# Optimization experiments

Hardware: AMD Instinct MI355X
Metric: run time of the kernel (lower is better)

## Reference

```python
import jax, jax.numpy as jnp
import numpy as np
import math

V, B, S, D, H, DH, DMEM = 32000, 4, 1024, 1024, 16, 64, 16
HD = H * DH  # == D (required by ff: Linear(n_head*d_head, d_model))
SCALE = 1.0 / math.sqrt(DH)


def pos_table(max_len, d):
    pos = jnp.arange(max_len, dtype=jnp.float32)[:, None]
    freqs = jnp.power(10000.0, -jnp.arange(0, d, 2, dtype=jnp.float32) / d)
    tab = jnp.zeros((max_len, d), dtype=jnp.float32)
    tab = tab.at[:, 0::2].set(jnp.sin(pos * freqs))
    tab = tab.at[:, 1::2].set(jnp.cos(pos * freqs))
    return tab


def layer_norm(x, g, b, eps=1e-5):
    mu = x.mean(-1, keepdims=True)
    var = ((x - mu) ** 2).mean(-1, keepdims=True)
    return (x - mu) * jax.lax.rsqrt(var + eps) * g + b


def mha(h, c, qw, kvw, ow, g, b):
    # h: [B,Sq,D] queries; c: [B,Skv,D] key/value source (post-lnorm, no mask, eval mode)
    q = (h @ qw).reshape(h.shape[0], h.shape[1], H, DH)
    k, v = jnp.split(c @ kvw, 2, axis=-1)
    k = k.reshape(c.shape[0], c.shape[1], H, DH)
    v = v.reshape(c.shape[0], c.shape[1], H, DH)
    scores = jnp.einsum('bind,bjnd->bijn', q, k) * SCALE
    probs = jax.nn.softmax(scores, axis=2)  # softmax over key axis j
    vec = jnp.einsum('bijn,bjnd->bind', probs, v).reshape(h.shape[0], h.shape[1], HD)
    return layer_norm(h + vec @ ow, g, b)


def setup_inputs():
    key = jax.random.key(0)
    ks = jax.random.split(key, 16)
    w = lambda k, shape: jax.random.normal(k, shape, dtype=jnp.float32) * 0.02
    ones = lambda: jnp.ones((D,), dtype=jnp.float32)
    zeros = lambda: jnp.zeros((D,), dtype=jnp.float32)
    return {
        'data': jax.random.randint(ks[0], (B, S), 0, V, dtype=jnp.int32),
        'mem': jnp.zeros((B, DMEM, D), dtype=jnp.float32),
        'emb': w(ks[1], (V, D)),
        'a_qw': w(ks[2], (D, HD)), 'a_kvw': w(ks[3], (D, 2 * HD)), 'a_ow': w(ks[4], (HD, D)),
        'a_g': ones(), 'a_b': zeros(),
        'u_qw': w(ks[5], (D, HD)), 'u_kvw': w(ks[6], (D, 2 * HD)), 'u_ow': w(ks[7], (HD, D)),
        'u_g': ones(), 'u_b': zeros(),
        'ffu_w': w(ks[8], (HD, D)), 'lnu_g': ones(), 'lnu_b': zeros(),
        'o_qw': w(ks[9], (D, HD)), 'o_kvw': w(ks[10], (D, 2 * HD)), 'o_ow': w(ks[11], (HD, D)),
        'o_g': ones(), 'o_b': zeros(),
        'ff2_w': w(ks[12], (HD, D)), 'ln1_g': ones(), 'ln1_b': zeros(),
        'ln2_g': ones(), 'ln2_b': zeros(),
    }


def reference(data, mem, emb, a_qw, a_kvw, a_ow, a_g, a_b,
              u_qw, u_kvw, u_ow, u_g, u_b, ffu_w, lnu_g, lnu_b,
              o_qw, o_kvw, o_ow, o_g, o_b, ff2_w, ln1_g, ln1_b, ln2_g, ln2_b):
    pos = pos_table(S, D)[None, :, :]  # [1,S,D]
    # embedding scale + sinusoidal positional encoding (dropout=0 in eval)
    hids = emb[data] * math.sqrt(D) + pos
    # layer self-attention (post-lnorm residual)
    hids = mha(hids, hids, a_qw, a_kvw, a_ow, a_g, a_b)
    # UpdateAttn: queries from hids, kv over [mem; hids]
    u = mha(hids, jnp.concatenate([mem, hids], axis=1), u_qw, u_kvw, u_ow, u_g, u_b)
    u = u + u @ ffu_w          # output += self.ff(output)
    u = layer_norm(u, lnu_g, lnu_b)
    u = u + (u + pos)          # output += pos_emb(output)
    # memory rollover: keep last d_mem positions of [new_mem; hids]
    new_mem = jnp.concatenate([u, hids], axis=1)[:, -DMEM:, :]
    # OutputAttn: hids attend over [new_mem; hids]
    attn_out = mha(hids, jnp.concatenate([new_mem, hids], axis=1), o_qw, o_kvw, o_ow, o_g, o_b)
    out_attn = layer_norm(hids + attn_out, ln1_g, ln1_b)
    output = layer_norm(out_attn @ ff2_w + out_attn, ln2_g, ln2_b)
    return (output, new_mem)
```

## Files before the change

kernel.cpp:

```cpp
#include <hip/hip_runtime.h>
#include <hip/hip_bf16.h>
#include <math.h>

typedef __bf16 bf16;
typedef __bf16 bf16x4 __attribute__((ext_vector_type(4)));
typedef __bf16 bf16x8 __attribute__((ext_vector_type(8)));
typedef float floatx4 __attribute__((ext_vector_type(4)));

#define LOG2E 1.44269504088896340736f
#define AS1 __attribute__((address_space(1)))
#define AS3 __attribute__((address_space(3)))

__device__ __forceinline__ void async_g2l16(const bf16* g, bf16* l) {
  __builtin_amdgcn_global_load_lds((AS1 void*)(void*)g, (AS3 void*)(void*)l, 16, 0, 0);
}

__global__ __launch_bounds__(256) void embed_kernel(const int* __restrict__ data,
                                                    const float* __restrict__ emb,
                                                    bf16* __restrict__ out) {
  int row = blockIdx.x;
  int s = row & 1023;
  int tok = data[row];
  int d = threadIdx.x * 4;
  floatx4 ev = *(const floatx4*)(emb + (size_t)tok * 1024 + d);
  bf16x4 ov;
#pragma unroll
  for (int i = 0; i < 4; i++) {
    int di = d + i;
    float e = -(float)(di & ~1) * (13.287712379549449f / 1024.0f);
    float freq = exp2f(e);
    float ang = (float)s * freq;
    float pv = (di & 1) ? cosf(ang) : sinf(ang);
    ov[i] = (bf16)(ev[i] * 32.0f + pv);
  }
  *(bf16x4*)(out + (size_t)row * 1024 + d) = ov;
}

__global__ __launch_bounds__(256) void transpose_kernel(const float* __restrict__ src,
                                                        bf16* __restrict__ dst,
                                                        int R, int C) {
  __shared__ __align__(16) bf16 tile[64][72];
  int c0 = blockIdx.x * 64, r0 = blockIdx.y * 64;
  int t = threadIdx.x;
  int r = t >> 2, cg = (t & 3) * 16;
  const float* sp = src + (size_t)(r0 + r) * C + c0 + cg;
  floatx4 f0 = *(const floatx4*)sp;
  floatx4 f1 = *(const floatx4*)(sp + 4);
  floatx4 f2 = *(const floatx4*)(sp + 8);
  floatx4 f3 = *(const floatx4*)(sp + 12);
  bf16x8 v0, v1;
#pragma unroll
  for (int i = 0; i < 4; i++) {
    v0[i] = (bf16)f0[i];
    v0[4 + i] = (bf16)f1[i];
    v1[i] = (bf16)f2[i];
    v1[4 + i] = (bf16)f3[i];
  }
  *(bf16x8*)&tile[r][cg] = v0;
  *(bf16x8*)&tile[r][cg + 8] = v1;
  __syncthreads();
  bf16x8 o0, o1;
#pragma unroll
  for (int i = 0; i < 8; i++) o0[i] = tile[cg + i][r];
#pragma unroll
  for (int i = 0; i < 8; i++) o1[i] = tile[cg + 8 + i][r];
  bf16* dp = dst + (size_t)(c0 + r) * R + r0 + cg;
  *(bf16x8*)dp = o0;
  *(bf16x8*)(dp + 8) = o1;
}

template <int EPI, int MT>
__global__ __launch_bounds__(256) void gemm_kernel(const bf16* __restrict__ A,
                                                   const bf16* __restrict__ Bt,
                                                   bf16* __restrict__ C0,
                                                   bf16* __restrict__ C1,
                                                   bf16* __restrict__ Vt, int N) {
  constexpr int NJ = (MT == 128) ? 4 : 2;
  constexpr int PA = MT / 32;
  __shared__ __align__(16) bf16 As[MT * 64];
  __shared__ __align__(16) bf16 Bs[128 * 64];
  const int K = 1024;
  int m0 = blockIdx.x * MT, n0 = blockIdx.y * 128;
  int t = threadIdx.x;
  int l = t & 63, w = t >> 6;
  int lr = l & 15, qd = l >> 4;
  int xorb = lr & 7;
  int wrow = __builtin_amdgcn_readfirstlane(t & 192);
  int wm = (MT == 128) ? (w & 1) : 0;
  int wn = (MT == 128) ? (w >> 1) : w;
  int mwbase = wm * 64;
  int nwbase = (MT == 128) ? (wn * 64) : (wn * 32);
  floatx4 acc[4][NJ] = {};
  for (int k0 = 0; k0 < K; k0 += 64) {
#pragma unroll
    for (int p = 0; p < PA; p++) {
      int jl = p * 256 + t;
      int r = jl >> 3;
      int bi = (jl & 7) ^ (r & 7);
      async_g2l16(A + (size_t)(m0 + r) * K + k0 + bi * 8, &As[(p * 256 + wrow) * 8]);
    }
#pragma unroll
    for (int p = 0; p < 4; p++) {
      int jl = p * 256 + t;
      int r = jl >> 3;
      int bi = (jl & 7) ^ (r & 7);
      async_g2l16(Bt + (size_t)(n0 + r) * K + k0 + bi * 8, &Bs[(p * 256 + wrow) * 8]);
    }
    __syncthreads();
#pragma unroll
    for (int c = 0; c < 2; c++) {
      bf16x8 fa[4], fb[NJ];
#pragma unroll
      for (int i = 0; i < 4; i++)
        fa[i] = *(const bf16x8*)&As[(mwbase + i * 16 + lr) * 64 + ((c * 4 + qd) ^ xorb) * 8];
#pragma unroll
      for (int j = 0; j < NJ; j++)
        fb[j] = *(const bf16x8*)&Bs[(nwbase + j * 16 + lr) * 64 + ((c * 4 + qd) ^ xorb) * 8];
#pragma unroll
      for (int i = 0; i < 4; i++)
#pragma unroll
        for (int j = 0; j < NJ; j++)
          acc[i][j] = __builtin_amdgcn_mfma_f32_16x16x32_bf16(fa[i], fb[j], acc[i][j], 0, 0, 0);
    }
    __syncthreads();
  }
#pragma unroll
  for (int i = 0; i < 4; i++) {
    int mbase = m0 + mwbase + i * 16 + qd * 4;
#pragma unroll
    for (int j = 0; j < NJ; j++) {
      int n = n0 + nwbase + j * 16 + lr;
      if (EPI == 0) {
#pragma unroll
        for (int r = 0; r < 4; r++)
          C0[(size_t)(mbase + r) * N + n] = (bf16)acc[i][j][r];
      } else {
        if (n < 1024) {
#pragma unroll
          for (int r = 0; r < 4; r++)
            C0[(size_t)(mbase + r) * 1024 + n] = (bf16)acc[i][j][r];
        } else if (n < 2048) {
#pragma unroll
          for (int r = 0; r < 4; r++)
            C1[(size_t)(mbase + r) * 1024 + (n - 1024)] = (bf16)acc[i][j][r];
        } else {
          int nn = n - 2048;
          int h = nn >> 6, d = nn & 63;
          int bb = mbase >> 10, s = mbase & 1023;
          bf16x4 v = {(bf16)acc[i][j][0], (bf16)acc[i][j][1],
                      (bf16)acc[i][j][2], (bf16)acc[i][j][3]};
          *(bf16x4*)(Vt + ((size_t)((bb * 16 + h) * 64 + d) << 10) + s) = v;
        }
      }
    }
  }
}

__global__ __launch_bounds__(256) void attn_kernel(const bf16* __restrict__ Q,
                                                   const bf16* __restrict__ Kb,
                                                   const bf16* __restrict__ Vt,
                                                   bf16* __restrict__ O,
                                                   int Skv, int memmode) {
  __shared__ __align__(16) bf16 Kt[2][64 * 64];
  __shared__ __align__(16) bf16 Vs[2][64 * 64];
  __shared__ __align__(16) bf16 P[4][16][72];
  int bid = blockIdx.x;
  int qb = bid & 15, h = (bid >> 4) & 15, b = bid >> 8;
  int t = threadIdx.x, w = t >> 6, l = t & 63;
  int lr = l & 15, qd = l >> 4;
  int xorb = lr & 7;
  int wrow = __builtin_amdgcn_readfirstlane(t & 192);
  int q0 = qb * 64 + w * 16;
  const bf16* Qrow = Q + (size_t)(b * 1024 + q0 + lr) * 1024 + h * 64;
  bf16x8 aq0 = *(const bf16x8*)(Qrow + qd * 8);
  bf16x8 aq1 = *(const bf16x8*)(Qrow + 32 + qd * 8);
  floatx4 Oacc[4] = {};
  float lsum[4] = {0.f, 0.f, 0.f, 0.f};
  const bf16* Kbase = Kb + (size_t)b * 1024 * 1024 + h * 64;
  const bf16* Vbase = Vt + (size_t)(b * 16 + h) * 64 * 1024;
  int nkt = (Skv + 63) >> 6;

  auto stage = [&](int kt, int bufi) {
    int j0 = kt * 64;
#pragma unroll
    for (int p = 0; p < 2; p++) {
      int jl = p * 256 + t;
      int kr = jl >> 3;
      int bi = (jl & 7) ^ (kr & 7);
      int key = j0 + kr;
      int kc = min(key, Skv - 1);
      int tok = memmode ? (kc < 16 ? 1008 + kc : kc - 16) : kc;
      async_g2l16(Kbase + (size_t)tok * 1024 + bi * 8, &Kt[bufi][(p * 256 + wrow) * 8]);
    }
#pragma unroll
    for (int p = 0; p < 2; p++) {
      int jl = p * 256 + t;
      int dr = jl >> 3;
      int bi = (jl & 7) ^ (dr & 7);
      int jb = j0 + bi * 8;
      int jbc = min(jb, Skv - 8);
      int tok = memmode ? (jbc < 16 ? 1008 + jbc : jbc - 16) : jbc;
      async_g2l16(Vbase + (size_t)dr * 1024 + tok, &Vs[bufi][(p * 256 + wrow) * 8]);
    }
  };

  stage(0, 0);
  for (int kt = 0; kt < nkt; kt++) {
    int buf = kt & 1;
    __syncthreads();
    if (kt + 1 < nkt) stage(kt + 1, buf ^ 1);
    int j0 = kt * 64;
    floatx4 sc[4] = {};
#pragma unroll
    for (int g = 0; g < 4; g++) {
      const bf16* kp = &Kt[buf][(g * 16 + lr) * 64];
      bf16x8 kb0 = *(const bf16x8*)(kp + ((qd ^ xorb) * 8));
      bf16x8 kb1 = *(const bf16x8*)(kp + (((4 + qd) ^ xorb) * 8));
      sc[g] = __builtin_amdgcn_mfma_f32_16x16x32_bf16(aq0, kb0, sc[g], 0, 0, 0);
      sc[g] = __builtin_amdgcn_mfma_f32_16x16x32_bf16(aq1, kb1, sc[g], 0, 0, 0);
    }
#pragma unroll
    for (int g = 0; g < 4; g++) {
      int key = j0 + g * 16 + lr;
      float msk = (key < Skv) ? 1.0f : 0.0f;
#pragma unroll
      for (int r = 0; r < 4; r++) {
        float p = exp2f(sc[g][r] * (0.125f * LOG2E)) * msk;
        lsum[r] += p;
        P[w][qd * 4 + r][g * 16 + lr] = (bf16)p;
      }
    }
#pragma unroll
    for (int c = 0; c < 2; c++) {
      bf16x8 ap = *(const bf16x8*)&P[w][lr][c * 32 + qd * 8];
#pragma unroll
      for (int tt = 0; tt < 4; tt++) {
        const bf16* vp = &Vs[buf][(tt * 16 + lr) * 64];
        bf16x8 vb = *(const bf16x8*)(vp + (((c * 4 + qd) ^ xorb) * 8));
        Oacc[tt] = __builtin_amdgcn_mfma_f32_16x16x32_bf16(ap, vb, Oacc[tt], 0, 0, 0);
      }
    }
  }
#pragma unroll
  for (int r = 0; r < 4; r++) {
    float s = lsum[r];
    s += __shfl_xor(s, 1);
    s += __shfl_xor(s, 2);
    s += __shfl_xor(s, 4);
    s += __shfl_xor(s, 8);
    lsum[r] = 1.0f / s;
  }
#pragma unroll
  for (int tt = 0; tt < 4; tt++)
#pragma unroll
    for (int r = 0; r < 4; r++) {
      size_t orow = (size_t)(b * 1024 + q0 + qd * 4 + r) * 1024 + h * 64 + tt * 16 + lr;
      O[orow] = (bf16)(Oacc[tt][r] * lsum[r]);
    }
}

template <typename OutT>
__global__ __launch_bounds__(256) void ln_kernel(const bf16* __restrict__ x,
                                                 const bf16* __restrict__ res,
                                                 const float* __restrict__ g,
                                                 const float* __restrict__ bta,
                                                 OutT* __restrict__ out) {
  __shared__ float red1[4], red2[4];
  int row = blockIdx.x, t = threadIdx.x;
  size_t base = (size_t)row * 1024 + t * 4;
  bf16x4 xv = *(const bf16x4*)(x + base);
  bf16x4 rv = *(const bf16x4*)(res + base);
  float v[4];
  float s = 0.f;
#pragma unroll
  for (int i = 0; i < 4; i++) {
    v[i] = (float)xv[i] + (float)rv[i];
    s += v[i];
  }
#pragma unroll
  for (int m = 32; m; m >>= 1) s += __shfl_xor(s, m);
  if ((t & 63) == 0) red1[t >> 6] = s;
  __syncthreads();
  float mu = (red1[0] + red1[1] + red1[2] + red1[3]) * (1.0f / 1024.0f);
  float sq = 0.f;
#pragma unroll
  for (int i = 0; i < 4; i++) {
    float dd = v[i] - mu;
    sq += dd * dd;
  }
#pragma unroll
  for (int m = 32; m; m >>= 1) sq += __shfl_xor(sq, m);
  if ((t & 63) == 0) red2[t >> 6] = sq;
  __syncthreads();
  float var = (red2[0] + red2[1] + red2[2] + red2[3]) * (1.0f / 1024.0f);
  float rs = rsqrtf(var + 1e-5f);
  floatx4 gv = *(const floatx4*)(g + t * 4);
  floatx4 bv = *(const floatx4*)(bta + t * 4);
  if constexpr (sizeof(OutT) == 2) {
    bf16x4 ov;
#pragma unroll
    for (int i = 0; i < 4; i++)
      ov[i] = (bf16)((v[i] - mu) * rs * gv[i] + bv[i]);
    *(bf16x4*)(out + base) = ov;
  } else {
    floatx4 ov;
#pragma unroll
    for (int i = 0; i < 4; i++)
      ov[i] = (v[i] - mu) * rs * gv[i] + bv[i];
    *(floatx4*)(out + base) = ov;
  }
}

__global__ __launch_bounds__(256) void copymem_kernel(const bf16* __restrict__ hids,
                                                      float* __restrict__ out) {
  int idx = blockIdx.x * 256 + threadIdx.x;
  int bb = idx >> 14;
  int r = (idx >> 10) & 15;
  int d = idx & 1023;
  out[idx] = (float)hids[((size_t)(bb * 1024 + 1008 + r) << 10) + d];
}

extern "C" void kernel_launch(void* const* d_in, const int* in_sizes, int n_in,
                              void* d_out, int out_size, void* d_ws, size_t ws_size,
                              hipStream_t stream) {
  const int* data = (const int*)d_in[0];
  const float* emb = (const float*)d_in[2];
  const float* a_qw = (const float*)d_in[3];
  const float* a_kvw = (const float*)d_in[4];
  const float* a_ow = (const float*)d_in[5];
  const float* a_g = (const float*)d_in[6];
  const float* a_b = (const float*)d_in[7];
  const float* o_qw = (const float*)d_in[16];
  const float* o_kvw = (const float*)d_in[17];
  const float* o_ow = (const float*)d_in[18];
  const float* o_g = (const float*)d_in[19];
  const float* o_b = (const float*)d_in[20];
  const float* ff2_w = (const float*)d_in[21];
  const float* ln1_g = (const float*)d_in[22];
  const float* ln1_b = (const float*)d_in[23];
  const float* ln2_g = (const float*)d_in[24];
  const float* ln2_b = (const float*)d_in[25];
  float* out = (float*)d_out;

  char* ws = (char*)d_ws;
  size_t off = 0;
  auto alloc = [&](size_t elems) {
    bf16* p = (bf16*)(ws + off);
    off += elems * 2;
    return p;
  };
  bf16* Wt_s1 = alloc(3072 * 1024);
  bf16* Wt_s2 = alloc(3072 * 1024);
  bf16* Wt_aow = alloc(1024 * 1024);
  bf16* Wt_oow = alloc(1024 * 1024);
  bf16* Wt_ff2 = alloc(1024 * 1024);
  bf16* hids0 = alloc(4096 * 1024);
  bf16* hids = alloc(4096 * 1024);
  bf16* Qb = alloc(4096 * 1024);
  bf16* Kb = alloc(4096 * 1024);
  bf16* Vtb = alloc(4096 * 1024);
  bf16* vecb = alloc(4096 * 1024);
  bf16* projb = Qb;
  bf16* attn_out = vecb;

  dim3 tb(256);
  transpose_kernel<<<dim3(16, 16), tb, 0, stream>>>(a_qw, Wt_s1, 1024, 1024);
  transpose_kernel<<<dim3(32, 16), tb, 0, stream>>>(a_kvw, Wt_s1 + 1024 * 1024, 1024, 2048);
  transpose_kernel<<<dim3(16, 16), tb, 0, stream>>>(o_qw, Wt_s2, 1024, 1024);
  transpose_kernel<<<dim3(32, 16), tb, 0, stream>>>(o_kvw, Wt_s2 + 1024 * 1024, 1024, 2048);
  transpose_kernel<<<dim3(16, 16), tb, 0, stream>>>(a_ow, Wt_aow, 1024, 1024);
  transpose_kernel<<<dim3(16, 16), tb, 0, stream>>>(o_ow, Wt_oow, 1024, 1024);
  transpose_kernel<<<dim3(16, 16), tb, 0, stream>>>(ff2_w, Wt_ff2, 1024, 1024);

  embed_kernel<<<4096, tb, 0, stream>>>(data, emb, hids0);

  gemm_kernel<1, 128><<<dim3(32, 24), tb, 0, stream>>>(hids0, Wt_s1, Qb, Kb, Vtb, 3072);
  attn_kernel<<<1024, tb, 0, stream>>>(Qb, Kb, Vtb, vecb, 1024, 0);
  gemm_kernel<0, 64><<<dim3(64, 8), tb, 0, stream>>>(vecb, Wt_aow, projb, nullptr, nullptr, 1024);
  ln_kernel<bf16><<<4096, tb, 0, stream>>>(projb, hids0, a_g, a_b, hids);

  gemm_kernel<1, 128><<<dim3(32, 24), tb, 0, stream>>>(hids, Wt_s2, Qb, Kb, Vtb, 3072);
  attn_kernel<<<1024, tb, 0, stream>>>(Qb, Kb, Vtb, vecb, 1040, 1);
  gemm_kernel<0, 64><<<dim3(64, 8), tb, 0, stream>>>(vecb, Wt_oow, projb, nullptr, nullptr, 1024);
  ln_kernel<bf16><<<4096, tb, 0, stream>>>(projb, hids, o_g, o_b, attn_out);
  ln_kernel<bf16><<<4096, tb, 0, stream>>>(attn_out, hids, ln1_g, ln1_b, hids0);

  gemm_kernel<0, 64><<<dim3(64, 8), tb, 0, stream>>>(hids0, Wt_ff2, projb, nullptr, nullptr, 1024);
  ln_kernel<float><<<4096, tb, 0, stream>>>(projb, hids0, ln2_g, ln2_b, out);

  copymem_kernel<<<256, tb, 0, stream>>>(hids, out + 4194304);
}
```

Baseline: 488.1 us.

## Fuse transposes, dual layernorm with mem copy, swizzle P, tune launch bounds

Merges the seven weight-transpose launches into a single 3D-grid launch, and fuses the two back-to-back layernorms with the new_mem copy into one kernel. This removes launch overhead and one intermediate round trip through global memory. It also swaps the padded P scratch in attention for an XOR-swizzled layout, adds occupancy hints to the gemm and attention kernels, and computes sin and cos together with the fast __sincosf intrinsic in the embedding. The fast intrinsic and the occupancy hints risk lower precision or register spills.

```diff
diff --git a/kernel.cpp b/kernel.cpp
--- a/kernel.cpp
+++ b/kernel.cpp
@@ -25,20 +25,30 @@
   floatx4 ev = *(const floatx4*)(emb + (size_t)tok * 1024 + d);
   bf16x4 ov;
 #pragma unroll
-  for (int i = 0; i < 4; i++) {
-    int di = d + i;
-    float e = -(float)(di & ~1) * (13.287712379549449f / 1024.0f);
+  for (int pr = 0; pr < 2; pr++) {
+    int di = d + pr * 2;
+    float e = -(float)di * (13.287712379549449f / 1024.0f);
     float freq = exp2f(e);
     float ang = (float)s * freq;
-    float pv = (di & 1) ? cosf(ang) : sinf(ang);
-    ov[i] = (bf16)(ev[i] * 32.0f + pv);
+    float sv, cv;
+    __sincosf(ang, &sv, &cv);
+    ov[pr * 2] = (bf16)(ev[pr * 2] * 32.0f + sv);
+    ov[pr * 2 + 1] = (bf16)(ev[pr * 2 + 1] * 32.0f + cv);
   }
   *(bf16x4*)(out + (size_t)row * 1024 + d) = ov;
 }
 
-__global__ __launch_bounds__(256) void transpose_kernel(const float* __restrict__ src,
-                                                        bf16* __restrict__ dst,
-                                                        int R, int C) {
+struct TransArgs {
+  const float* src[7];
+  bf16* dst[7];
+  int cblk[7];
+};
+__global__ __launch_bounds__(256) void transpose_all_kernel(TransArgs a) {
+  int z = blockIdx.z;
+  if ((int)blockIdx.x >= a.cblk[z]) return;
+  const float* __restrict__ src = a.src[z];
+  bf16* __restrict__ dst = a.dst[z];
+  int C = a.cblk[z] * 64;
   __shared__ __align__(16) bf16 tile[64][72];
   int c0 = blockIdx.x * 64, r0 = blockIdx.y * 64;
   int t = threadIdx.x;
@@ -64,17 +74,17 @@
   for (int i = 0; i < 8; i++) o0[i] = tile[cg + i][r];
 #pragma unroll
   for (int i = 0; i < 8; i++) o1[i] = tile[cg + 8 + i][r];
-  bf16* dp = dst + (size_t)(c0 + r) * R + r0 + cg;
+  bf16* dp = dst + (size_t)(c0 + r) * 1024 + r0 + cg;
   *(bf16x8*)dp = o0;
   *(bf16x8*)(dp + 8) = o1;
 }
 
 template <int EPI, int MT>
-__global__ __launch_bounds__(256) void gemm_kernel(const bf16* __restrict__ A,
-                                                   const bf16* __restrict__ Bt,
-                                                   bf16* __restrict__ C0,
-                                                   bf16* __restrict__ C1,
-                                                   bf16* __restrict__ Vt, int N) {
+__global__ __launch_bounds__(256, 3) void gemm_kernel(const bf16* __restrict__ A,
+                                                      const bf16* __restrict__ Bt,
+                                                      bf16* __restrict__ C0,
+                                                      bf16* __restrict__ C1,
+                                                      bf16* __restrict__ Vt, int N) {
   constexpr int NJ = (MT == 128) ? 4 : 2;
   constexpr int PA = MT / 32;
   __shared__ __align__(16) bf16 As[MT * 64];
@@ -156,20 +166,21 @@
   }
 }
 
-__global__ __launch_bounds__(256) void attn_kernel(const bf16* __restrict__ Q,
-                                                   const bf16* __restrict__ Kb,
-                                                   const bf16* __restrict__ Vt,
-                                                   bf16* __restrict__ O,
-                                                   int Skv, int memmode) {
+__global__ __launch_bounds__(256, 4) void attn_kernel(const bf16* __restrict__ Q,
+                                                      const bf16* __restrict__ Kb,
+                                                      const bf16* __restrict__ Vt,
+                                                      bf16* __restrict__ O,
+                                                      int Skv, int memmode) {
   __shared__ __align__(16) bf16 Kt[2][64 * 64];
   __shared__ __align__(16) bf16 Vs[2][64 * 64];
-  __shared__ __align__(16) bf16 P[4][16][72];
+  __shared__ __align__(16) bf16 Ps[4 * 16 * 64];
   int bid = blockIdx.x;
   int qb = bid & 15, h = (bid >> 4) & 15, b = bid >> 8;
   int t = threadIdx.x, w = t >> 6, l = t & 63;
   int lr = l & 15, qd = l >> 4;
   int xorb = lr & 7;
   int wrow = __builtin_amdgcn_readfirstlane(t & 192);
+  int pw = w << 10;
   int q0 = qb * 64 + w * 16;
   const bf16* Qrow = Q + (size_t)(b * 1024 + q0 + lr) * 1024 + h * 64;
   bf16x8 aq0 = *(const bf16x8*)(Qrow + qd * 8);
@@ -223,20 +234,24 @@
     for (int g = 0; g < 4; g++) {
       int key = j0 + g * 16 + lr;
       float msk = (key < Skv) ? 1.0f : 0.0f;
+      int bcol = (g << 1) | (lr >> 3);
+      int c7 = lr & 7;
 #pragma unroll
       for (int r = 0; r < 4; r++) {
+        int prow = qd * 4 + r;
         float p = exp2f(sc[g][r] * (0.125f * LOG2E)) * msk;
         lsum[r] += p;
-        P[w][qd * 4 + r][g * 16 + lr] = (bf16)p;
+        Ps[pw + prow * 64 + (((bcol ^ (prow & 7)) << 3) | c7)] = (bf16)p;
       }
     }
 #pragma unroll
     for (int c = 0; c < 2; c++) {
-      bf16x8 ap = *(const bf16x8*)&P[w][lr][c * 32 + qd * 8];
+      int cb = c * 4 + qd;
+      bf16x8 ap = *(const bf16x8*)&Ps[pw + lr * 64 + ((cb ^ (lr & 7)) << 3)];
 #pragma unroll
       for (int tt = 0; tt < 4; tt++) {
         const bf16* vp = &Vs[buf][(tt * 16 + lr) * 64];
-        bf16x8 vb = *(const bf16x8*)(vp + (((c * 4 + qd) ^ xorb) * 8));
+        bf16x8 vb = *(const bf16x8*)(vp + ((cb ^ xorb) * 8));
         Oacc[tt] = __builtin_amdgcn_mfma_f32_16x16x32_bf16(ap, vb, Oacc[tt], 0, 0, 0);
       }
     }
@@ -311,13 +326,84 @@
   }
 }
 
-__global__ __launch_bounds__(256) void copymem_kernel(const bf16* __restrict__ hids,
-                                                      float* __restrict__ out) {
-  int idx = blockIdx.x * 256 + threadIdx.x;
-  int bb = idx >> 14;
-  int r = (idx >> 10) & 15;
-  int d = idx & 1023;
-  out[idx] = (float)hids[((size_t)(bb * 1024 + 1008 + r) << 10) + d];
+__global__ __launch_bounds__(256) void dualln_kernel(const bf16* __restrict__ x,
+                                                     const bf16* __restrict__ hids,
+                                                     const float* __restrict__ g1,
+                                                     const float* __restrict__ b1,
+                                                     const float* __restrict__ g2,
+                                                     const float* __restrict__ b2,
+                                                     bf16* __restrict__ out,
+                                                     float* __restrict__ newmem) {
+  __shared__ float ra[4], rb[4], rc[4], rd[4];
+  int row = blockIdx.x, t = threadIdx.x;
+  size_t base = (size_t)row * 1024 + t * 4;
+  bf16x4 xv = *(const bf16x4*)(x + base);
+  bf16x4 hv = *(const bf16x4*)(hids + base);
+  float hf[4], v[4];
+  float s = 0.f;
+#pragma unroll
+  for (int i = 0; i < 4; i++) {
+    hf[i] = (float)hv[i];
+    v[i] = (float)xv[i] + hf[i];
+    s += v[i];
+  }
+  int ss = row & 1023;
+  if (ss >= 1008) {
+    int bb = row >> 10;
+    floatx4 mv = {hf[0], hf[1], hf[2], hf[3]};
+    *(floatx4*)(newmem + ((size_t)(bb * 16 + ss - 1008) << 10) + t * 4) = mv;
+  }
+#pragma unroll
+  for (int m = 32; m; m >>= 1) s += __shfl_xor(s, m);
+  if ((t & 63) == 0) ra[t >> 6] = s;
+  __syncthreads();
+  float mu = (ra[0] + ra[1] + ra[2] + ra[3]) * (1.0f / 1024.0f);
+  float sq = 0.f;
+#pragma unroll
+  for (int i = 0; i < 4; i++) {
+    float dd = v[i] - mu;
+    sq += dd * dd;
+  }
+#pragma unroll
+  for (int m = 32; m; m >>= 1) sq += __shfl_xor(sq, m);
+  if ((t & 63) == 0) rb[t >> 6] = sq;
+  __syncthreads();
+  float var = (rb[0] + rb[1] + rb[2] + rb[3]) * (1.0f / 1024.0f);
+  float rs = rsqrtf(var + 1e-5f);
+  floatx4 g1v = *(const floatx4*)(g1 + t * 4);
+  floatx4 b1v = *(const floatx4*)(b1 + t * 4);
+  float y[4];
+  float s2 = 0.f;
+#pragma unroll
+  for (int i = 0; i < 4; i++) {
+    float a = (v[i] - mu) * rs * g1v[i] + b1v[i];
+    y[i] = hf[i] + a;
+    s2 += y[i];
+  }
+#pragma unroll
+  for (int m = 32; m; m >>= 1) s2 += __shfl_xor(s2, m);
+  if ((t & 63) == 0) rc[t >> 6] = s2;
+  __syncthreads();
+  float mu2 = (rc[0] + rc[1] + rc[2] + rc[3]) * (1.0f / 1024.0f);
+  float sq2 = 0.f;
+#pragma unroll
+  for (int i = 0; i < 4; i++) {
+    float dd = y[i] - mu2;
+    sq2 += dd * dd;
+  }
+#pragma unroll
+  for (int m = 32; m; m >>= 1) sq2 += __shfl_xor(sq2, m);
+  if ((t & 63) == 0) rd[t >> 6] = sq2;
+  __syncthreads();
+  float var2 = (rd[0] + rd[1] + rd[2] + rd[3]) * (1.0f / 1024.0f);
+  float rs2 = rsqrtf(var2 + 1e-5f);
+  floatx4 g2v = *(const floatx4*)(g2 + t * 4);
+  floatx4 b2v = *(const floatx4*)(b2 + t * 4);
+  bf16x4 ov;
+#pragma unroll
+  for (int i = 0; i < 4; i++)
+    ov[i] = (bf16)((y[i] - mu2) * rs2 * g2v[i] + b2v[i]);
+  *(bf16x4*)(out + base) = ov;
 }
 
 extern "C" void kernel_launch(void* const* d_in, const int* in_sizes, int n_in,
@@ -361,16 +447,17 @@
   bf16* Vtb = alloc(4096 * 1024);
   bf16* vecb = alloc(4096 * 1024);
   bf16* projb = Qb;
-  bf16* attn_out = vecb;
 
   dim3 tb(256);
-  transpose_kernel<<<dim3(16, 16), tb, 0, stream>>>(a_qw, Wt_s1, 1024, 1024);
-  transpose_kernel<<<dim3(32, 16), tb, 0, stream>>>(a_kvw, Wt_s1 + 1024 * 1024, 1024, 2048);
-  transpose_kernel<<<dim3(16, 16), tb, 0, stream>>>(o_qw, Wt_s2, 1024, 1024);
-  transpose_kernel<<<dim3(32, 16), tb, 0, stream>>>(o_kvw, Wt_s2 + 1024 * 1024, 1024, 2048);
-  transpose_kernel<<<dim3(16, 16), tb, 0, stream>>>(a_ow, Wt_aow, 1024, 1024);
-  transpose_kernel<<<dim3(16, 16), tb, 0, stream>>>(o_ow, Wt_oow, 1024, 1024);
-  transpose_kernel<<<dim3(16, 16), tb, 0, stream>>>(ff2_w, Wt_ff2, 1024, 1024);
+  TransArgs ta;
+  ta.src[0] = a_qw;  ta.dst[0] = Wt_s1;               ta.cblk[0] = 16;
+  ta.src[1] = a_kvw; ta.dst[1] = Wt_s1 + 1024 * 1024; ta.cblk[1] = 32;
+  ta.src[2] = o_qw;  ta.dst[2] = Wt_s2;               ta.cblk[2] = 16;
+  ta.src[3] = o_kvw; ta.dst[3] = Wt_s2 + 1024 * 1024; ta.cblk[3] = 32;
+  ta.src[4] = a_ow;  ta.dst[4] = Wt_aow;              ta.cblk[4] = 16;
+  ta.src[5] = o_ow;  ta.dst[5] = Wt_oow;              ta.cblk[5] = 16;
+  ta.src[6] = ff2_w; ta.dst[6] = Wt_ff2;              ta.cblk[6] = 16;
+  transpose_all_kernel<<<dim3(32, 16, 7), tb, 0, stream>>>(ta);
 
   embed_kernel<<<4096, tb, 0, stream>>>(data, emb, hids0);
 
@@ -382,11 +469,9 @@
   gemm_kernel<1, 128><<<dim3(32, 24), tb, 0, stream>>>(hids, Wt_s2, Qb, Kb, Vtb, 3072);
   attn_kernel<<<1024, tb, 0, stream>>>(Qb, Kb, Vtb, vecb, 1040, 1);
   gemm_kernel<0, 64><<<dim3(64, 8), tb, 0, stream>>>(vecb, Wt_oow, projb, nullptr, nullptr, 1024);
-  ln_kernel<bf16><<<4096, tb, 0, stream>>>(projb, hids, o_g, o_b, attn_out);
-  ln_kernel<bf16><<<4096, tb, 0, stream>>>(attn_out, hids, ln1_g, ln1_b, hids0);
+  dualln_kernel<<<4096, tb, 0, stream>>>(projb, hids, o_g, o_b, ln1_g, ln1_b, hids0,
+                                         out + 4194304);
 
   gemm_kernel<0, 64><<<dim3(64, 8), tb, 0, stream>>>(hids0, Wt_ff2, projb, nullptr, nullptr, 1024);
   ln_kernel<float><<<4096, tb, 0, stream>>>(projb, hids0, ln2_g, ln2_b, out);
-
-  copymem_kernel<<<256, tb, 0, stream>>>(hids, out + 4194304);
-}
+}
```

Result: faster. 455.2 us (-6.8%).
